# Performance work log

Hardware: AMD Instinct MI355X
Metric: run time of the kernel (lower is better)

## Reference

```python
import jax, jax.numpy as jnp
import numpy as np

WINDOW_SIZE = 7
C1 = 0.01 ** 2
C2 = 0.03 ** 2


def _gaussian_window(ws: int) -> jnp.ndarray:
    sigma = ws / 6.0
    coords = jnp.arange(ws, dtype=jnp.float32) - ws // 2
    g = jnp.exp(-coords ** 2 / (2 * sigma ** 2))
    g = g / g.sum()
    k3 = g[:, None, None] * g[None, :, None] * g[None, None, :]
    k3 = k3 / k3.sum()
    return k3.reshape(1, 1, ws, ws, ws)  # OIDHW


def _conv3d_same(x, w):
    pad = WINDOW_SIZE // 2
    return jax.lax.conv_general_dilated(
        x, w, window_strides=(1, 1, 1),
        padding=[(pad, pad)] * 3,
        dimension_numbers=('NCDHW', 'OIDHW', 'NCDHW'))


def setup_inputs() -> dict:
    key = jax.random.key(0)
    k1, k2 = jax.random.split(key)
    shape = (2, 1, 160, 160, 160)
    predicted = jax.random.uniform(k1, shape, dtype=jnp.float32)
    target = jax.random.uniform(k2, shape, dtype=jnp.float32)
    return {"predicted": predicted, "target": target}


def reference(predicted, target):
    window = _gaussian_window(WINDOW_SIZE)
    mu1 = _conv3d_same(predicted, window)
    mu2 = _conv3d_same(target, window)
    mu1_sq = mu1 ** 2
    mu2_sq = mu2 ** 2
    mu1_mu2 = mu1 * mu2
    sigma1_sq = _conv3d_same(predicted ** 2, window) - mu1_sq
    sigma2_sq = _conv3d_same(target ** 2, window) - mu2_sq
    sigma12 = _conv3d_same(predicted * target, window) - mu1_mu2
    ssim_map = ((2 * mu1_mu2 + C1) * (2 * sigma12 + C2)) / (
        (mu1_sq + mu2_sq + C1) * (sigma1_sq + sigma2_sq + C2))
    return 1.0 - ssim_map.mean()
```

## Files before the change

kernel.cpp:

```cpp
#include <hip/hip_runtime.h>
#include <math.h>

#define DD 160
#define HH 160
#define WW 160
#define NB 2
#define NEL (NB*DD*HH*WW)

#define XT 32
#define YT 16
#define ZC 16
#define NTHR 256
#define NZCH (DD/ZC)
#define GX (WW/XT)
#define GY (HH/YT)
#define NPART (GX*GY*NB*NZCH)

#define HR 22
#define CP 35

struct G7 { float g[7]; };

__device__ __forceinline__ float2 f2fma(float s, float2 a, float2 b) {
    return make_float2(fmaf(s, a.x, b.x), fmaf(s, a.y, b.y));
}

__global__ __launch_bounds__(NTHR, 4) void ssim_fused(
        const float* __restrict__ p, const float* __restrict__ t,
        float* __restrict__ partial, G7 gw) {
    const int tid = threadIdx.x;
    const int tx  = tid & 31;
    const int tyo = tid >> 5;
    const int x0 = blockIdx.x * XT;
    const int y0 = blockIdx.y * YT;
    const int n  = blockIdx.z / NZCH;
    const int zs = (blockIdx.z % NZCH) * ZC;

    __shared__ float4 c4[2][HR][CP];

    float2 r01[2][6], r23[2][6];
#pragma unroll
    for (int yo = 0; yo < 2; ++yo)
#pragma unroll
        for (int j = 0; j < 6; ++j) {
            r01[yo][j] = make_float2(0.f, 0.f);
            r23[yo][j] = make_float2(0.f, 0.f);
        }

    const float C1v = 1e-4f, C2v = 9e-4f;
    float ssum = 0.f;
    const int hw = HH * WW;
    const float* pv = p + (size_t)n * DD * hw;
    const float* tv = t + (size_t)n * DD * hw;

    const int br = tid >> 3;
    const int bxg = tid & 7;
    const int bgy = y0 + br - 3;
    const bool browok = (unsigned)bgy < (unsigned)HH && tid < HR * 8;
    const int cbase = x0 + 4 * bxg - 4;
    const int pcr = tx + (tx >> 3);

    for (int s = zs - 3; s < zs + ZC + 3; ++s) {
        const int par = s & 1;
        float2 m01[2], m23[2];
#pragma unroll
        for (int yo = 0; yo < 2; ++yo) {
            m01[yo] = make_float2(0.f, 0.f);
            m23[yo] = make_float2(0.f, 0.f);
        }

        const bool valid = (s >= 0) && (s < DD);
        if (valid) {
            if (tid < HR * 8) {
                const float* prow = pv + (size_t)s * hw + bgy * WW;
                const float* trow = tv + (size_t)s * hw + bgy * WW;
                float2 pt[12], qu[12];
#pragma unroll
                for (int q = 0; q < 3; ++q) {
                    int c0 = cbase + 4 * q;
                    float4 a = make_float4(0.f, 0.f, 0.f, 0.f);
                    float4 b = a;
                    if (browok && (unsigned)c0 < (unsigned)WW) {
                        a = *(const float4*)(prow + c0);
                        b = *(const float4*)(trow + c0);
                    }
                    float u, d;
                    pt[4*q+0] = make_float2(a.x, b.x);
                    u = a.x + b.x; d = a.x - b.x;
                    qu[4*q+0] = make_float2(u * u, d * d);
                    pt[4*q+1] = make_float2(a.y, b.y);
                    u = a.y + b.y; d = a.y - b.y;
                    qu[4*q+1] = make_float2(u * u, d * d);
                    pt[4*q+2] = make_float2(a.z, b.z);
                    u = a.z + b.z; d = a.z - b.z;
                    qu[4*q+2] = make_float2(u * u, d * d);
                    pt[4*q+3] = make_float2(a.w, b.w);
                    u = a.w + b.w; d = a.w - b.w;
                    qu[4*q+3] = make_float2(u * u, d * d);
                }
#pragma unroll
                for (int e = 0; e < 4; ++e) {
                    float2 s01 = make_float2(0.f, 0.f);
                    float2 s23 = make_float2(0.f, 0.f);
#pragma unroll
                    for (int k = 0; k < 7; ++k) {
                        float w = gw.g[k];
                        s01 = f2fma(w, pt[e + k + 1], s01);
                        s23 = f2fma(w, qu[e + k + 1], s23);
                    }
                    int c = 4 * bxg + e;
                    c4[par][br][c + (c >> 3)] =
                        make_float4(s01.x, s01.y, s23.x, s23.y);
                }
            }
            __syncthreads();

#pragma unroll
            for (int r8 = 0; r8 < 8; ++r8) {
                float4 v = c4[par][2 * tyo + r8][pcr];
                float2 v01 = make_float2(v.x, v.y);
                float2 v23 = make_float2(v.z, v.w);
                if (r8 < 7) {
                    float w = gw.g[r8];
                    m01[0] = f2fma(w, v01, m01[0]);
                    m23[0] = f2fma(w, v23, m23[0]);
                }
                if (r8 > 0) {
                    float w = gw.g[r8 - 1];
                    m01[1] = f2fma(w, v01, m01[1]);
                    m23[1] = f2fma(w, v23, m23[1]);
                }
            }
        }

        float2 cons01[2], cons23[2];
#pragma unroll
        for (int yo = 0; yo < 2; ++yo) {
            float2 v01 = m01[yo], v23 = m23[yo];
            cons01[yo] = f2fma(gw.g[6], v01, r01[yo][0]);
            cons23[yo] = f2fma(gw.g[6], v23, r23[yo][0]);
#pragma unroll
            for (int j = 0; j < 5; ++j) {
                r01[yo][j] = f2fma(gw.g[5 - j], v01, r01[yo][j + 1]);
                r23[yo][j] = f2fma(gw.g[5 - j], v23, r23[yo][j + 1]);
            }
            r01[yo][5] = make_float2(gw.g[0] * v01.x, gw.g[0] * v01.y);
            r23[yo][5] = make_float2(gw.g[0] * v23.x, gw.g[0] * v23.y);
        }

        if (s >= zs + 3) {
#pragma unroll
            for (int yo = 0; yo < 2; ++yo) {
                float mu1 = cons01[yo].x, mu2 = cons01[yo].y;
                float Eu  = cons23[yo].x, Ew  = cons23[yo].y;
                float mu12 = mu1 * mu2, mu1sq = mu1 * mu1, mu2sq = mu2 * mu2;
                float sumsq = 0.5f  * (Eu + Ew) - mu1sq - mu2sq;
                float s12   = 0.25f * (Eu - Ew) - mu12;
                float num = (2.f * mu12 + C1v) * (2.f * s12 + C2v);
                float den = (mu1sq + mu2sq + C1v) * (sumsq + C2v);
                ssum += num * __builtin_amdgcn_rcpf(den);
            }
        }
    }

#pragma unroll
    for (int off = 32; off > 0; off >>= 1)
        ssum += __shfl_down(ssum, off, 64);
    __shared__ float wsum[4];
    if ((tid & 63) == 0) wsum[tid >> 6] = ssum;
    __syncthreads();
    if (tid == 0) {
        int bid = (blockIdx.z * GY + blockIdx.y) * GX + blockIdx.x;
        partial[bid] = wsum[0] + wsum[1] + wsum[2] + wsum[3];
    }
}

__global__ __launch_bounds__(256) void ssim_final(
        const float* __restrict__ partial, float* __restrict__ out) {
    float s = 0.f;
    for (int i = threadIdx.x; i < NPART; i += 256) s += partial[i];
#pragma unroll
    for (int off = 32; off > 0; off >>= 1)
        s += __shfl_down(s, off, 64);
    __shared__ float wsum[4];
    int lane = threadIdx.x & 63, wid = threadIdx.x >> 6;
    if (lane == 0) wsum[wid] = s;
    __syncthreads();
    if (threadIdx.x == 0) {
        float tot = wsum[0] + wsum[1] + wsum[2] + wsum[3];
        out[0] = 1.0f - tot / (float)NEL;
    }
}

extern "C" void kernel_launch(void* const* d_in, const int* in_sizes, int n_in,
                              void* d_out, int out_size, void* d_ws, size_t ws_size,
                              hipStream_t stream) {
    const float* p = (const float*)d_in[0];
    const float* t = (const float*)d_in[1];
    float* out = (float*)d_out;
    float* partial = (float*)d_ws;

    G7 gw;
    {
        double s = 0.0, sig = 7.0 / 6.0;
        double g[7];
        for (int i = 0; i < 7; ++i) {
            double d = (double)i - 3.0;
            g[i] = exp(-d * d / (2.0 * sig * sig));
            s += g[i];
        }
        for (int i = 0; i < 7; ++i) gw.g[i] = (float)(g[i] / s);
    }

    dim3 grid(GX, GY, NB * NZCH);
    ssim_fused<<<grid, NTHR, 0, stream>>>(p, t, partial, gw);
    ssim_final<<<1, 256, 0, stream>>>(partial, out);
}
```

Baseline: 136.2 us.

## Enlarge Y tile to 32 rows with four outputs per thread and packed float2 math

Doubles the block's Y tile from 16 to 32 rows, so each thread now produces four vertically adjacent outputs instead of two. This cuts the 6-row halo overhead in X-filtered rows and global loads per output, with two rounds of row jobs per thread to cover the 38 halo rows. It also switches to ext_vector_type float2 arithmetic so the compiler can emit packed FMA instructions, and fuses the X-pass accumulation into the load loop. In exchange it roughly doubles the z-ring registers per thread (NY*6*2 v2f), which may reduce occupancy under launch_bounds(256,4), and it halves the number of blocks.

New measurement: 146.4 us. +7.5%, slower.

```diff
diff --git a/kernel.cpp b/kernel.cpp
--- a/kernel.cpp
+++ b/kernel.cpp
@@ -8,7 +8,8 @@
 #define NEL (NB*DD*HH*WW)
 
 #define XT 32
-#define YT 16
+#define YT 32
+#define NY 4
 #define ZC 16
 #define NTHR 256
 #define NZCH (DD/ZC)
@@ -16,14 +17,13 @@
 #define GY (HH/YT)
 #define NPART (GX*GY*NB*NZCH)
 
-#define HR 22
+#define HR 38
+#define NJOB (HR*8)
 #define CP 35
 
+typedef float v2f __attribute__((ext_vector_type(2)));
+
 struct G7 { float g[7]; };
-
-__device__ __forceinline__ float2 f2fma(float s, float2 a, float2 b) {
-    return make_float2(fmaf(s, a.x, b.x), fmaf(s, a.y, b.y));
-}
 
 __global__ __launch_bounds__(NTHR, 4) void ssim_fused(
         const float* __restrict__ p, const float* __restrict__ t,
@@ -38,13 +38,13 @@
 
     __shared__ float4 c4[2][HR][CP];
 
-    float2 r01[2][6], r23[2][6];
-#pragma unroll
-    for (int yo = 0; yo < 2; ++yo)
+    v2f r01[NY][6], r23[NY][6];
+#pragma unroll
+    for (int yo = 0; yo < NY; ++yo)
 #pragma unroll
         for (int j = 0; j < 6; ++j) {
-            r01[yo][j] = make_float2(0.f, 0.f);
-            r23[yo][j] = make_float2(0.f, 0.f);
+            r01[yo][j] = (v2f)(0.f);
+            r23[yo][j] = (v2f)(0.f);
         }
 
     const float C1v = 1e-4f, C2v = 9e-4f;
@@ -53,106 +53,106 @@
     const float* pv = p + (size_t)n * DD * hw;
     const float* tv = t + (size_t)n * DD * hw;
 
-    const int br = tid >> 3;
-    const int bxg = tid & 7;
-    const int bgy = y0 + br - 3;
-    const bool browok = (unsigned)bgy < (unsigned)HH && tid < HR * 8;
-    const int cbase = x0 + 4 * bxg - 4;
+    const int br0 = tid >> 3, bxg0 = tid & 7;
+    const int br1 = (tid + NTHR) >> 3, bxg1 = tid & 7;
     const int pcr = tx + (tx >> 3);
 
     for (int s = zs - 3; s < zs + ZC + 3; ++s) {
         const int par = s & 1;
-        float2 m01[2], m23[2];
-#pragma unroll
-        for (int yo = 0; yo < 2; ++yo) {
-            m01[yo] = make_float2(0.f, 0.f);
-            m23[yo] = make_float2(0.f, 0.f);
-        }
 
         const bool valid = (s >= 0) && (s < DD);
+        v2f m01[NY], m23[NY];
         if (valid) {
-            if (tid < HR * 8) {
-                const float* prow = pv + (size_t)s * hw + bgy * WW;
-                const float* trow = tv + (size_t)s * hw + bgy * WW;
-                float2 pt[12], qu[12];
-#pragma unroll
-                for (int q = 0; q < 3; ++q) {
-                    int c0 = cbase + 4 * q;
-                    float4 a = make_float4(0.f, 0.f, 0.f, 0.f);
-                    float4 b = a;
-                    if (browok && (unsigned)c0 < (unsigned)WW) {
-                        a = *(const float4*)(prow + c0);
-                        b = *(const float4*)(trow + c0);
+            const float* pz = pv + (size_t)s * hw;
+            const float* tz = tv + (size_t)s * hw;
+
+#pragma unroll
+            for (int rnd = 0; rnd < 2; ++rnd) {
+                const int br  = rnd ? br1 : br0;
+                const int bxg = rnd ? bxg1 : bxg0;
+                if (rnd == 0 || tid < NJOB - NTHR) {
+                    const int gy = y0 + br - 3;
+                    const bool rowok = (unsigned)gy < (unsigned)HH;
+                    const float* prow = pz + gy * WW;
+                    const float* trow = tz + gy * WW;
+                    const int cbase = x0 + 4 * bxg - 4;
+                    v2f s01[4], s23[4];
+#pragma unroll
+                    for (int e = 0; e < 4; ++e) { s01[e] = (v2f)(0.f); s23[e] = (v2f)(0.f); }
+#pragma unroll
+                    for (int q = 0; q < 3; ++q) {
+                        int c0 = cbase + 4 * q;
+                        float4 a = make_float4(0.f, 0.f, 0.f, 0.f);
+                        float4 b = a;
+                        if (rowok && (unsigned)c0 < (unsigned)WW) {
+                            a = *(const float4*)(prow + c0);
+                            b = *(const float4*)(trow + c0);
+                        }
+                        const float af[4] = {a.x, a.y, a.z, a.w};
+                        const float bf[4] = {b.x, b.y, b.z, b.w};
+#pragma unroll
+                        for (int j = 0; j < 4; ++j) {
+                            const int i = 4 * q + j;
+                            v2f pt; pt[0] = af[j]; pt[1] = bf[j];
+                            v2f ud; ud[0] = af[j] + bf[j]; ud[1] = af[j] - bf[j];
+                            v2f qu = ud * ud;
+#pragma unroll
+                            for (int e = 0; e < 4; ++e) {
+                                const int k = i - e - 1;
+                                if (k >= 0 && k < 7) {
+                                    s01[e] = gw.g[k] * pt + s01[e];
+                                    s23[e] = gw.g[k] * qu + s23[e];
+                                }
+                            }
+                        }
                     }
-                    float u, d;
-                    pt[4*q+0] = make_float2(a.x, b.x);
-                    u = a.x + b.x; d = a.x - b.x;
-                    qu[4*q+0] = make_float2(u * u, d * d);
-                    pt[4*q+1] = make_float2(a.y, b.y);
-                    u = a.y + b.y; d = a.y - b.y;
-                    qu[4*q+1] = make_float2(u * u, d * d);
-                    pt[4*q+2] = make_float2(a.z, b.z);
-                    u = a.z + b.z; d = a.z - b.z;
-                    qu[4*q+2] = make_float2(u * u, d * d);
-                    pt[4*q+3] = make_float2(a.w, b.w);
-                    u = a.w + b.w; d = a.w - b.w;
-                    qu[4*q+3] = make_float2(u * u, d * d);
+#pragma unroll
+                    for (int e = 0; e < 4; ++e) {
+                        int c = 4 * bxg + e;
+                        c4[par][br][c + (c >> 3)] =
+                            make_float4(s01[e][0], s01[e][1], s23[e][0], s23[e][1]);
+                    }
                 }
-#pragma unroll
-                for (int e = 0; e < 4; ++e) {
-                    float2 s01 = make_float2(0.f, 0.f);
-                    float2 s23 = make_float2(0.f, 0.f);
-#pragma unroll
-                    for (int k = 0; k < 7; ++k) {
-                        float w = gw.g[k];
-                        s01 = f2fma(w, pt[e + k + 1], s01);
-                        s23 = f2fma(w, qu[e + k + 1], s23);
+            }
+            __syncthreads();
+
+#pragma unroll
+            for (int yo = 0; yo < NY; ++yo) { m01[yo] = (v2f)(0.f); m23[yo] = (v2f)(0.f); }
+#pragma unroll
+            for (int r10 = 0; r10 < 10; ++r10) {
+                float4 v = c4[par][4 * tyo + r10][pcr];
+                v2f v01; v01[0] = v.x; v01[1] = v.y;
+                v2f v23; v23[0] = v.z; v23[1] = v.w;
+#pragma unroll
+                for (int yo = 0; yo < NY; ++yo) {
+                    const int k = r10 - yo;
+                    if (k >= 0 && k < 7) {
+                        m01[yo] = gw.g[k] * v01 + m01[yo];
+                        m23[yo] = gw.g[k] * v23 + m23[yo];
                     }
-                    int c = 4 * bxg + e;
-                    c4[par][br][c + (c >> 3)] =
-                        make_float4(s01.x, s01.y, s23.x, s23.y);
                 }
             }
-            __syncthreads();
-
-#pragma unroll
-            for (int r8 = 0; r8 < 8; ++r8) {
-                float4 v = c4[par][2 * tyo + r8][pcr];
-                float2 v01 = make_float2(v.x, v.y);
-                float2 v23 = make_float2(v.z, v.w);
-                if (r8 < 7) {
-                    float w = gw.g[r8];
-                    m01[0] = f2fma(w, v01, m01[0]);
-                    m23[0] = f2fma(w, v23, m23[0]);
-                }
-                if (r8 > 0) {
-                    float w = gw.g[r8 - 1];
-                    m01[1] = f2fma(w, v01, m01[1]);
-                    m23[1] = f2fma(w, v23, m23[1]);
-                }
-            }
-        }
-
-        float2 cons01[2], cons23[2];
-#pragma unroll
-        for (int yo = 0; yo < 2; ++yo) {
-            float2 v01 = m01[yo], v23 = m23[yo];
-            cons01[yo] = f2fma(gw.g[6], v01, r01[yo][0]);
-            cons23[yo] = f2fma(gw.g[6], v23, r23[yo][0]);
+        } else {
+#pragma unroll
+            for (int yo = 0; yo < NY; ++yo) { m01[yo] = (v2f)(0.f); m23[yo] = (v2f)(0.f); }
+        }
+
+#pragma unroll
+        for (int yo = 0; yo < NY; ++yo) {
+            v2f v01 = m01[yo], v23 = m23[yo];
+            v2f cons01 = gw.g[6] * v01 + r01[yo][0];
+            v2f cons23 = gw.g[6] * v23 + r23[yo][0];
 #pragma unroll
             for (int j = 0; j < 5; ++j) {
-                r01[yo][j] = f2fma(gw.g[5 - j], v01, r01[yo][j + 1]);
-                r23[yo][j] = f2fma(gw.g[5 - j], v23, r23[yo][j + 1]);
-            }
-            r01[yo][5] = make_float2(gw.g[0] * v01.x, gw.g[0] * v01.y);
-            r23[yo][5] = make_float2(gw.g[0] * v23.x, gw.g[0] * v23.y);
-        }
-
-        if (s >= zs + 3) {
-#pragma unroll
-            for (int yo = 0; yo < 2; ++yo) {
-                float mu1 = cons01[yo].x, mu2 = cons01[yo].y;
-                float Eu  = cons23[yo].x, Ew  = cons23[yo].y;
+                r01[yo][j] = gw.g[5 - j] * v01 + r01[yo][j + 1];
+                r23[yo][j] = gw.g[5 - j] * v23 + r23[yo][j + 1];
+            }
+            r01[yo][5] = gw.g[0] * v01;
+            r23[yo][5] = gw.g[0] * v23;
+
+            if (s >= zs + 3) {
+                float mu1 = cons01[0], mu2 = cons01[1];
+                float Eu  = cons23[0], Ew  = cons23[1];
                 float mu12 = mu1 * mu2, mu1sq = mu1 * mu1, mu2sq = mu2 * mu2;
                 float sumsq = 0.5f  * (Eu + Ew) - mu1sq - mu2sq;
                 float s12   = 0.25f * (Eu - Ew) - mu12;
@@ -166,12 +166,15 @@
 #pragma unroll
     for (int off = 32; off > 0; off >>= 1)
         ssum += __shfl_down(ssum, off, 64);
-    __shared__ float wsum[4];
+    __shared__ float wsum[8];
     if ((tid & 63) == 0) wsum[tid >> 6] = ssum;
     __syncthreads();
     if (tid == 0) {
+        float tot = 0.f;
+#pragma unroll
+        for (int w = 0; w < 8; ++w) tot += wsum[w];
         int bid = (blockIdx.z * GY + blockIdx.y) * GX + blockIdx.x;
-        partial[bid] = wsum[0] + wsum[1] + wsum[2] + wsum[3];
+        partial[bid] = tot;
     }
 }
 
```
